# Performance work log

Hardware: AMD Instinct MI355X
Metric: run time of the kernel (lower is better)

Reference implementation:

```python
import jax, jax.numpy as jnp
import numpy as np

PATCH = 7
STRIDE = 1
PDIM = 3 * PATCH * PATCH  # 147


def _extract_patches(im):
    # torch.nn.Unfold(kernel=7, stride=1): output [b, c*k*k, L] with channel-major
    # ordering, which matches conv_general_dilated_patches' channel-major layout.
    b = im.shape[0]
    p = jax.lax.conv_general_dilated_patches(
        im, filter_shape=(PATCH, PATCH), window_strides=(STRIDE, STRIDE), padding='VALID'
    )  # [b, 147, h', w']
    p = p.reshape(b, PDIM, -1).transpose(0, 2, 1)  # [b, L, 147]
    # normalize_patch='mean': std_mean over ALL dims, only the mean is subtracted
    return p - p.mean()


def setup_inputs() -> dict:
    key = jax.random.key(0)
    k1, k2, k3, k4, k5 = jax.random.split(key, 5)
    B, C, H, W = 16, 3, 128, 128
    L = ((H - PATCH) // STRIDE + 1) ** 2  # 14884
    n_samples, n_proj = 4096, 128
    x = jax.random.normal(k1, (B, C, H, W), dtype=jnp.float32)
    y = jax.random.normal(k2, (B, C, H, W), dtype=jnp.float32)
    # faithful quirk: sample_same_locations=True re-draws a fresh permutation for y
    idx_x = jax.random.permutation(k3, L)[:n_samples].astype(jnp.int32)
    idx_y = jax.random.permutation(k4, L)[:n_samples].astype(jnp.int32)
    proj = jax.random.normal(k5, (PDIM, n_proj), dtype=jnp.float32)
    proj = proj / jnp.linalg.norm(proj, axis=0, keepdims=True)  # unit-norm slices
    return {"x": x, "y": y, "proj": proj, "idx_x": idx_x, "idx_y": idx_y}


def reference(x, y, proj, idx_x, idx_y):
    xp = _extract_patches(x)[:, idx_x]  # [b, n, 147]
    yp = _extract_patches(y)[:, idx_y]  # [b, n, 147]
    # SWD dist_metric, vectorized over the batch dim (replaces the Python loop):
    # project patches onto random unit directions, sort along the sample axis,
    # mean absolute difference of sorted projections.
    px = jnp.sort(jnp.einsum('bnd,dp->bnp', xp, proj), axis=1)  # [b, n, P]
    py = jnp.sort(jnp.einsum('bnd,dp->bnp', yp, proj), axis=1)
    per_sample = jnp.mean(jnp.abs(px - py), axis=(1, 2))  # [b]
    return per_sample.mean()  # batch_reduction='mean'
```

## Files before the change

### kernel.cpp

```cpp
#include <hip/hip_runtime.h>
#include <cstddef>
#include <cstdint>

#define BATCH 16
#define CHAN 3
#define HH 128
#define WW 128
#define PATCHK 7
#define HP 122
#define PDIM 147
#define NSAMP 4096
#define NPROJ 128
#define IMG_PIX (CHAN*HH*WW)
#define TOT_PIX (BATCH*IMG_PIX)
#define COUNT_D ((double)BATCH*HP*HP*PDIM)

__global__ __launch_bounds__(256)
void k_wsum(const float* __restrict__ x, const float* __restrict__ y,
            double* __restrict__ outx, double* __restrict__ outy) {
  float sx = 0.f, sy = 0.f;
  const int stride = gridDim.x * blockDim.x;
  for (int e = blockIdx.x * blockDim.x + threadIdx.x; e < TOT_PIX; e += stride) {
    int j = e & (WW - 1);
    int i = (e >> 7) & (HH - 1);
    int wi = min(i, HP - 1) - max(0, i - (PATCHK - 1)) + 1;
    int wj = min(j, HP - 1) - max(0, j - (PATCHK - 1)) + 1;
    float w = (float)(wi * wj);
    sx = fmaf(x[e], w, sx);
    sy = fmaf(y[e], w, sy);
  }
  __shared__ float rx[256], ry[256];
  const int tid = threadIdx.x;
  rx[tid] = sx; ry[tid] = sy;
  __syncthreads();
  for (int off = 128; off; off >>= 1) {
    if (tid < off) { rx[tid] += rx[tid + off]; ry[tid] += ry[tid + off]; }
    __syncthreads();
  }
  if (tid == 0) { outx[blockIdx.x] = (double)rx[0]; outy[blockIdx.x] = (double)ry[0]; }
}

__global__ void k_meandiff(const double* __restrict__ px, const double* __restrict__ py,
                           double* __restrict__ dmean) {
  __shared__ double s[256];
  const int tid = threadIdx.x;
  s[tid] = px[tid] - py[tid];
  __syncthreads();
  for (int off = 128; off; off >>= 1) {
    if (tid < off) s[tid] += s[tid + off];
    __syncthreads();
  }
  if (tid == 0) dmean[0] = s[0] / COUNT_D;
}

__global__ void k_colsum(const float* __restrict__ proj, float* __restrict__ sp) {
  const int p = threadIdx.x;
  float s = 0.f;
  for (int d = 0; d < PDIM; ++d) s += proj[d * NPROJ + p];
  sp[p] = s;
}

#define TM 64
#define ASTR (TM + 1)
__global__ __launch_bounds__(256)
void k_proj(const float* __restrict__ x, const float* __restrict__ y,
            const float* __restrict__ proj,
            const int* __restrict__ idx_x, const int* __restrict__ idx_y,
            float* __restrict__ PX, float* __restrict__ PY) {
  __shared__ float As[PDIM * ASTR];

  const int z = blockIdx.z;
  const float* im = z ? y : x;
  const int* idx = z ? idx_y : idx_x;
  float* dst = z ? PY : PX;
  const int b = blockIdx.y;
  const int nbase = blockIdx.x * TM;
  const int tid = threadIdx.x;

  const float* imb = im + b * IMG_PIX;
  for (int e = tid; e < TM * PDIM; e += 256) {
    int n = e / PDIM;
    int d = e - n * PDIM;
    int l = idx[nbase + n];
    int h0 = l / HP;
    int w0 = l - h0 * HP;
    int c  = d / 49;
    int r  = d - c * 49;
    int kh = r / 7;
    int kw = r - kh * 7;
    As[d * ASTR + n] = imb[(c * HH + h0 + kh) * WW + w0 + kw];
  }
  __syncthreads();

  const int lane = tid & 63;
  const int w = __builtin_amdgcn_readfirstlane(tid >> 6);
  const float* bp = proj + w * 32;

  float acc[32];
#pragma unroll
  for (int pp = 0; pp < 32; ++pp) acc[pp] = 0.f;

  for (int k = 0; k < PDIM; ++k) {
    const float a = As[k * ASTR + lane];
#pragma unroll
    for (int pp = 0; pp < 32; ++pp)
      acc[pp] = fmaf(a, bp[k * NPROJ + pp], acc[pp]);
  }

#pragma unroll
  for (int pp = 0; pp < 32; ++pp)
    dst[(size_t)(b * NPROJ + w * 32 + pp) * NSAMP + nbase + lane] = acc[pp];
}

#define CSWAP(a, b, u) { float _lo = fminf(a, b), _hi = fmaxf(a, b); \
                         (a) = (u) ? _lo : _hi; (b) = (u) ? _hi : _lo; }

#define PHASEA(v, u8) do { \
  CSWAP(v[0], v[1], true);  CSWAP(v[2], v[3], false); \
  CSWAP(v[4], v[5], true);  CSWAP(v[6], v[7], false); \
  CSWAP(v[0], v[2], true);  CSWAP(v[1], v[3], true);  \
  CSWAP(v[4], v[6], false); CSWAP(v[5], v[7], false); \
  CSWAP(v[0], v[1], true);  CSWAP(v[2], v[3], true);  \
  CSWAP(v[4], v[5], false); CSWAP(v[6], v[7], false); \
  CSWAP(v[0], v[4], u8); CSWAP(v[1], v[5], u8); \
  CSWAP(v[2], v[6], u8); CSWAP(v[3], v[7], u8); \
  CSWAP(v[0], v[2], u8); CSWAP(v[1], v[3], u8); \
  CSWAP(v[4], v[6], u8); CSWAP(v[5], v[7], u8); \
  CSWAP(v[0], v[1], u8); CSWAP(v[2], v[3], u8); \
  CSWAP(v[4], v[5], u8); CSWAP(v[6], v[7], u8); } while (0)

#define REG3(v, up) do { \
  CSWAP(v[0], v[4], up); CSWAP(v[1], v[5], up); \
  CSWAP(v[2], v[6], up); CSWAP(v[3], v[7], up); \
  CSWAP(v[0], v[2], up); CSWAP(v[1], v[3], up); \
  CSWAP(v[4], v[6], up); CSWAP(v[5], v[7], up); \
  CSWAP(v[0], v[1], up); CSWAP(v[2], v[3], up); \
  CSWAP(v[4], v[5], up); CSWAP(v[6], v[7], up); } while (0)

template <int DL>
__device__ __forceinline__ void shufstage(float (&vx)[8], float (&vy)[8],
                                          int t, bool up) {
  const bool keepLo = (((t & DL) == 0) == up);
#pragma unroll
  for (int r = 0; r < 8; ++r) {
    float ox = __shfl_xor(vx[r], DL, 64);
    vx[r] = keepLo ? fminf(vx[r], ox) : fmaxf(vx[r], ox);
    float oy = __shfl_xor(vy[r], DL, 64);
    vy[r] = keepLo ? fminf(vy[r], oy) : fmaxf(vy[r], oy);
  }
}

template <int K>
__device__ __forceinline__ void merge_inwave(float (&vx)[8], float (&vy)[8],
                                             int t, int ib) {
  const bool up = ((ib & K) == 0);
  if (K / 2 >= 256) shufstage<32>(vx, vy, t, up);
  if (K / 2 >= 128) shufstage<16>(vx, vy, t, up);
  if (K / 2 >= 64)  shufstage<8>(vx, vy, t, up);
  if (K / 2 >= 32)  shufstage<4>(vx, vy, t, up);
  if (K / 2 >= 16)  shufstage<2>(vx, vy, t, up);
  if (K / 2 >= 8)   shufstage<1>(vx, vy, t, up);
  REG3(vx, up);
  REG3(vy, up);
}

__device__ __forceinline__ void lds_stage(float (&vx)[8], float (&vy)[8],
                                          float* lx, float* ly, int t, int dl, bool up) {
  ((float4*)lx)[t * 2]     = make_float4(vx[0], vx[1], vx[2], vx[3]);
  ((float4*)lx)[t * 2 + 1] = make_float4(vx[4], vx[5], vx[6], vx[7]);
  ((float4*)ly)[t * 2]     = make_float4(vy[0], vy[1], vy[2], vy[3]);
  ((float4*)ly)[t * 2 + 1] = make_float4(vy[4], vy[5], vy[6], vy[7]);
  __syncthreads();
  const int pt = (t ^ dl) * 2;
  float4 ox0 = ((const float4*)lx)[pt], ox1 = ((const float4*)lx)[pt + 1];
  float4 oy0 = ((const float4*)ly)[pt], oy1 = ((const float4*)ly)[pt + 1];
  const bool kl = (((t & dl) == 0) == up);
  vx[0] = kl ? fminf(vx[0], ox0.x) : fmaxf(vx[0], ox0.x);
  vx[1] = kl ? fminf(vx[1], ox0.y) : fmaxf(vx[1], ox0.y);
  vx[2] = kl ? fminf(vx[2], ox0.z) : fmaxf(vx[2], ox0.z);
  vx[3] = kl ? fminf(vx[3], ox0.w) : fmaxf(vx[3], ox0.w);
  vx[4] = kl ? fminf(vx[4], ox1.x) : fmaxf(vx[4], ox1.x);
  vx[5] = kl ? fminf(vx[5], ox1.y) : fmaxf(vx[5], ox1.y);
  vx[6] = kl ? fminf(vx[6], ox1.z) : fmaxf(vx[6], ox1.z);
  vx[7] = kl ? fminf(vx[7], ox1.w) : fmaxf(vx[7], ox1.w);
  vy[0] = kl ? fminf(vy[0], oy0.x) : fmaxf(vy[0], oy0.x);
  vy[1] = kl ? fminf(vy[1], oy0.y) : fmaxf(vy[1], oy0.y);
  vy[2] = kl ? fminf(vy[2], oy0.z) : fmaxf(vy[2], oy0.z);
  vy[3] = kl ? fminf(vy[3], oy0.w) : fmaxf(vy[3], oy0.w);
  vy[4] = kl ? fminf(vy[4], oy1.x) : fmaxf(vy[4], oy1.x);
  vy[5] = kl ? fminf(vy[5], oy1.y) : fmaxf(vy[5], oy1.y);
  vy[6] = kl ? fminf(vy[6], oy1.z) : fmaxf(vy[6], oy1.z);
  vy[7] = kl ? fminf(vy[7], oy1.w) : fmaxf(vy[7], oy1.w);
  __syncthreads();
}

__global__ __launch_bounds__(512)
void k_sortdiff(const float* __restrict__ PX, const float* __restrict__ PY,
                const float* __restrict__ sp, const double* __restrict__ dmean,
                float* __restrict__ bsum) {
  __shared__ float lx[NSAMP];
  __shared__ float ly[NSAMP];
  __shared__ float red[8];
  const int bp = blockIdx.x;
  const int p = bp & (NPROJ - 1);
  const int t = threadIdx.x;
  const int ib = t * 8;

  float vx[8], vy[8];
  {
    const float4* rx = (const float4*)(PX + (size_t)bp * NSAMP) + t * 2;
    const float4* ry = (const float4*)(PY + (size_t)bp * NSAMP) + t * 2;
    float4 x0 = rx[0], x1 = rx[1], y0 = ry[0], y1 = ry[1];
    vx[0]=x0.x; vx[1]=x0.y; vx[2]=x0.z; vx[3]=x0.w;
    vx[4]=x1.x; vx[5]=x1.y; vx[6]=x1.z; vx[7]=x1.w;
    vy[0]=y0.x; vy[1]=y0.y; vy[2]=y0.z; vy[3]=y0.w;
    vy[4]=y1.x; vy[5]=y1.y; vy[6]=y1.z; vy[7]=y1.w;
  }

  {
    const bool u8 = ((t & 1) == 0);
    PHASEA(vx, u8);
    PHASEA(vy, u8);
  }

  merge_inwave<16>(vx, vy, t, ib);
  merge_inwave<32>(vx, vy, t, ib);
  merge_inwave<64>(vx, vy, t, ib);
  merge_inwave<128>(vx, vy, t, ib);
  merge_inwave<256>(vx, vy, t, ib);
  merge_inwave<512>(vx, vy, t, ib);

  {
    const bool up = ((ib & 1024) == 0);
    lds_stage(vx, vy, lx, ly, t, 512 >> 3, up);
    merge_inwave<1024>(vx, vy, t, ib);
  }
  {
    const bool up = ((ib & 2048) == 0);
    lds_stage(vx, vy, lx, ly, t, 1024 >> 3, up);
    lds_stage(vx, vy, lx, ly, t, 512 >> 3, up);
    merge_inwave<2048>(vx, vy, t, ib);
  }
  {
    const bool up = true;
    lds_stage(vx, vy, lx, ly, t, 2048 >> 3, up);
    lds_stage(vx, vy, lx, ly, t, 1024 >> 3, up);
    lds_stage(vx, vy, lx, ly, t, 512 >> 3, up);
    merge_inwave<4096>(vx, vy, t, ib);
  }

  const float delta = (float)(dmean[0]) * sp[p];
  float s = 0.f;
#pragma unroll
  for (int r = 0; r < 8; ++r) s += fabsf(vx[r] - vy[r] - delta);

#pragma unroll
  for (int o = 1; o < 64; o <<= 1) s += __shfl_xor(s, o, 64);
  if ((t & 63) == 0) red[t >> 6] = s;
  __syncthreads();
  if (t == 0) {
    float tot = 0.f;
#pragma unroll
    for (int i = 0; i < 8; ++i) tot += red[i];
    bsum[bp] = tot;
  }
}

__global__ void k_final(const float* __restrict__ bsum, float* __restrict__ out) {
  __shared__ double s[256];
  const int tid = threadIdx.x;
  double v = 0.0;
  for (int q = tid; q < BATCH * NPROJ; q += 256) v += (double)bsum[q];
  s[tid] = v;
  __syncthreads();
  for (int off = 128; off; off >>= 1) {
    if (tid < off) s[tid] += s[tid + off];
    __syncthreads();
  }
  if (tid == 0) out[0] = (float)(s[0] / ((double)NSAMP * NPROJ * BATCH));
}

extern "C" void kernel_launch(void* const* d_in, const int* in_sizes, int n_in,
                              void* d_out, int out_size, void* d_ws, size_t ws_size,
                              hipStream_t stream) {
  const float* x    = (const float*)d_in[0];
  const float* y    = (const float*)d_in[1];
  const float* proj = (const float*)d_in[2];
  const int* idx_x  = (const int*)d_in[3];
  const int* idx_y  = (const int*)d_in[4];
  float* out = (float*)d_out;

  char* ws = (char*)d_ws;
  double* pAx   = (double*)(ws + 0);
  double* pAy   = (double*)(ws + 2048);
  double* dmean = (double*)(ws + 4096);
  float*  sp    = (float*)(ws + 4160);
  float*  bsum  = (float*)(ws + 8192);
  float*  PX    = (float*)(ws + 16384);
  float*  PY    = PX + (size_t)BATCH * NPROJ * NSAMP;

  const size_t need = 16384 + 2ull * BATCH * NPROJ * NSAMP * sizeof(float);
  if (ws_size < need) return;

  k_wsum    <<<256, 256, 0, stream>>>(x, y, pAx, pAy);
  k_meandiff<<<1, 256, 0, stream>>>(pAx, pAy, dmean);
  k_colsum  <<<1, NPROJ, 0, stream>>>(proj, sp);
  k_proj    <<<dim3(NSAMP / TM, BATCH, 2), 256, 0, stream>>>(x, y, proj, idx_x, idx_y, PX, PY);
  k_sortdiff<<<BATCH * NPROJ, 512, 0, stream>>>(PX, PY, sp, dmean, bsum);
  k_final   <<<1, 256, 0, stream>>>(bsum, out);
}
```

Measured before the change: 266.3 us.

## Use sign-flip bitonic sort, DS swizzles, B-register double buffering, fused colsum

The bitonic sort now handles descending runs by XOR-flipping sign bits before and after each merge stage, so every compare-swap becomes a plain min/max instead of a direction-dependent select. Shuffles with lane distance 16 or less use ds_swizzle instead of the generic shfl_xor. The projection GEMM double-buffers the projection-row loads in registers, and the column-sum kernel is folded into the mean-difference kernel to save a launch. The sign-flip trick relies on an order-reversing bit mapping, and the larger register arrays could lower occupancy in k_proj.

```diff
diff --git a/kernel.cpp b/kernel.cpp
--- a/kernel.cpp
+++ b/kernel.cpp
@@ -41,27 +41,35 @@
 }
 
 __global__ void k_meandiff(const double* __restrict__ px, const double* __restrict__ py,
-                           double* __restrict__ dmean) {
-  __shared__ double s[256];
+                           double* __restrict__ dmean,
+                           const float* __restrict__ proj, float* __restrict__ sp) {
   const int tid = threadIdx.x;
-  s[tid] = px[tid] - py[tid];
+  if (tid < NPROJ) {
+    float s = 0.f;
+    for (int d = 0; d < PDIM; ++d) s += proj[d * NPROJ + tid];
+    sp[tid] = s;
+  }
+  __shared__ double sd[256];
+  sd[tid] = px[tid] - py[tid];
   __syncthreads();
   for (int off = 128; off; off >>= 1) {
-    if (tid < off) s[tid] += s[tid + off];
+    if (tid < off) sd[tid] += sd[tid + off];
     __syncthreads();
   }
-  if (tid == 0) dmean[0] = s[0] / COUNT_D;
-}
-
-__global__ void k_colsum(const float* __restrict__ proj, float* __restrict__ sp) {
-  const int p = threadIdx.x;
-  float s = 0.f;
-  for (int d = 0; d < PDIM; ++d) s += proj[d * NPROJ + p];
-  sp[p] = s;
+  if (tid == 0) dmean[0] = sd[0] / COUNT_D;
 }
 
 #define TM 64
 #define ASTR (TM + 1)
+__device__ __forceinline__ void loadb(float (&dst)[32], const float* bp, int kk) {
+#pragma unroll
+  for (int pp = 0; pp < 32; ++pp) dst[pp] = bp[kk * NPROJ + pp];
+}
+__device__ __forceinline__ void fma32(float a, const float (&b)[32], float (&acc)[32]) {
+#pragma unroll
+  for (int pp = 0; pp < 32; ++pp) acc[pp] = fmaf(a, b[pp], acc[pp]);
+}
+
 __global__ __launch_bounds__(256)
 void k_proj(const float* __restrict__ x, const float* __restrict__ y,
             const float* __restrict__ proj,
@@ -100,11 +108,19 @@
 #pragma unroll
   for (int pp = 0; pp < 32; ++pp) acc[pp] = 0.f;
 
-  for (int k = 0; k < PDIM; ++k) {
-    const float a = As[k * ASTR + lane];
-#pragma unroll
-    for (int pp = 0; pp < 32; ++pp)
-      acc[pp] = fmaf(a, bp[k * NPROJ + pp], acc[pp]);
+  float bA[32], bB[32];
+  loadb(bA, bp, 0);
+  for (int k = 0; k + 2 < PDIM; k += 2) {
+    loadb(bB, bp, k + 1);
+    const float a0 = As[k * ASTR + lane];
+    const float a1 = As[(k + 1) * ASTR + lane];
+    fma32(a0, bA, acc);
+    loadb(bA, bp, k + 2);
+    fma32(a1, bB, acc);
+  }
+  {
+    const float a = As[146 * ASTR + lane];
+    fma32(a, bA, acc);
   }
 
 #pragma unroll
@@ -112,60 +128,51 @@
     dst[(size_t)(b * NPROJ + w * 32 + pp) * NSAMP + nbase + lane] = acc[pp];
 }
 
-#define CSWAP(a, b, u) { float _lo = fminf(a, b), _hi = fmaxf(a, b); \
-                         (a) = (u) ? _lo : _hi; (b) = (u) ? _hi : _lo; }
-
-#define PHASEA(v, u8) do { \
-  CSWAP(v[0], v[1], true);  CSWAP(v[2], v[3], false); \
-  CSWAP(v[4], v[5], true);  CSWAP(v[6], v[7], false); \
-  CSWAP(v[0], v[2], true);  CSWAP(v[1], v[3], true);  \
-  CSWAP(v[4], v[6], false); CSWAP(v[5], v[7], false); \
-  CSWAP(v[0], v[1], true);  CSWAP(v[2], v[3], true);  \
-  CSWAP(v[4], v[5], false); CSWAP(v[6], v[7], false); \
-  CSWAP(v[0], v[4], u8); CSWAP(v[1], v[5], u8); \
-  CSWAP(v[2], v[6], u8); CSWAP(v[3], v[7], u8); \
-  CSWAP(v[0], v[2], u8); CSWAP(v[1], v[3], u8); \
-  CSWAP(v[4], v[6], u8); CSWAP(v[5], v[7], u8); \
-  CSWAP(v[0], v[1], u8); CSWAP(v[2], v[3], u8); \
-  CSWAP(v[4], v[5], u8); CSWAP(v[6], v[7], u8); } while (0)
-
-#define REG3(v, up) do { \
-  CSWAP(v[0], v[4], up); CSWAP(v[1], v[5], up); \
-  CSWAP(v[2], v[6], up); CSWAP(v[3], v[7], up); \
-  CSWAP(v[0], v[2], up); CSWAP(v[1], v[3], up); \
-  CSWAP(v[4], v[6], up); CSWAP(v[5], v[7], up); \
-  CSWAP(v[0], v[1], up); CSWAP(v[2], v[3], up); \
-  CSWAP(v[4], v[5], up); CSWAP(v[6], v[7], up); } while (0)
+__device__ __forceinline__ float xorf(float v, unsigned m) {
+  return __int_as_float(__float_as_int(v) ^ (int)m);
+}
+#define CSW(a, b) { float _t = fminf(a, b); b = fmaxf(a, b); a = _t; }
+
+#define SORT8A(v) do { \
+  CSW(v[0],v[1]); CSW(v[3],v[2]); CSW(v[4],v[5]); CSW(v[7],v[6]); \
+  CSW(v[0],v[2]); CSW(v[1],v[3]); CSW(v[6],v[4]); CSW(v[7],v[5]); \
+  CSW(v[0],v[1]); CSW(v[2],v[3]); CSW(v[5],v[4]); CSW(v[7],v[6]); \
+  CSW(v[0],v[4]); CSW(v[1],v[5]); CSW(v[2],v[6]); CSW(v[3],v[7]); \
+  CSW(v[0],v[2]); CSW(v[1],v[3]); CSW(v[4],v[6]); CSW(v[5],v[7]); \
+  CSW(v[0],v[1]); CSW(v[2],v[3]); CSW(v[4],v[5]); CSW(v[6],v[7]); } while (0)
+
+#define REG3A(v) do { \
+  CSW(v[0],v[4]); CSW(v[1],v[5]); CSW(v[2],v[6]); CSW(v[3],v[7]); \
+  CSW(v[0],v[2]); CSW(v[1],v[3]); CSW(v[4],v[6]); CSW(v[5],v[7]); \
+  CSW(v[0],v[1]); CSW(v[2],v[3]); CSW(v[4],v[5]); CSW(v[6],v[7]); } while (0)
+
+#define FLIP8(v, m) { v[0]=xorf(v[0],m); v[1]=xorf(v[1],m); v[2]=xorf(v[2],m); \
+  v[3]=xorf(v[3],m); v[4]=xorf(v[4],m); v[5]=xorf(v[5],m); v[6]=xorf(v[6],m); \
+  v[7]=xorf(v[7],m); }
 
 template <int DL>
-__device__ __forceinline__ void shufstage(float (&vx)[8], float (&vy)[8],
-                                          int t, bool up) {
-  const bool keepLo = (((t & DL) == 0) == up);
+__device__ __forceinline__ float swzxor(float v) {
+  if constexpr (DL <= 16) {
+    return __int_as_float(
+        __builtin_amdgcn_ds_swizzle(__float_as_int(v), (DL << 10) | 0x1F));
+  } else {
+    return __shfl_xor(v, DL, 64);
+  }
+}
+
+template <int DL>
+__device__ __forceinline__ void shufxy(float (&vx)[8], float (&vy)[8], bool keepLo) {
 #pragma unroll
   for (int r = 0; r < 8; ++r) {
-    float ox = __shfl_xor(vx[r], DL, 64);
+    float ox = swzxor<DL>(vx[r]);
     vx[r] = keepLo ? fminf(vx[r], ox) : fmaxf(vx[r], ox);
-    float oy = __shfl_xor(vy[r], DL, 64);
+    float oy = swzxor<DL>(vy[r]);
     vy[r] = keepLo ? fminf(vy[r], oy) : fmaxf(vy[r], oy);
   }
 }
 
-template <int K>
-__device__ __forceinline__ void merge_inwave(float (&vx)[8], float (&vy)[8],
-                                             int t, int ib) {
-  const bool up = ((ib & K) == 0);
-  if (K / 2 >= 256) shufstage<32>(vx, vy, t, up);
-  if (K / 2 >= 128) shufstage<16>(vx, vy, t, up);
-  if (K / 2 >= 64)  shufstage<8>(vx, vy, t, up);
-  if (K / 2 >= 32)  shufstage<4>(vx, vy, t, up);
-  if (K / 2 >= 16)  shufstage<2>(vx, vy, t, up);
-  if (K / 2 >= 8)   shufstage<1>(vx, vy, t, up);
-  REG3(vx, up);
-  REG3(vy, up);
-}
-
 __device__ __forceinline__ void lds_stage(float (&vx)[8], float (&vy)[8],
-                                          float* lx, float* ly, int t, int dl, bool up) {
+                                          float* lx, float* ly, int t, int dl, bool kl) {
   ((float4*)lx)[t * 2]     = make_float4(vx[0], vx[1], vx[2], vx[3]);
   ((float4*)lx)[t * 2 + 1] = make_float4(vx[4], vx[5], vx[6], vx[7]);
   ((float4*)ly)[t * 2]     = make_float4(vy[0], vy[1], vy[2], vy[3]);
@@ -174,7 +181,6 @@
   const int pt = (t ^ dl) * 2;
   float4 ox0 = ((const float4*)lx)[pt], ox1 = ((const float4*)lx)[pt + 1];
   float4 oy0 = ((const float4*)ly)[pt], oy1 = ((const float4*)ly)[pt + 1];
-  const bool kl = (((t & dl) == 0) == up);
   vx[0] = kl ? fminf(vx[0], ox0.x) : fmaxf(vx[0], ox0.x);
   vx[1] = kl ? fminf(vx[1], ox0.y) : fmaxf(vx[1], ox0.y);
   vx[2] = kl ? fminf(vx[2], ox0.z) : fmaxf(vx[2], ox0.z);
@@ -203,8 +209,23 @@
   __shared__ float red[8];
   const int bp = blockIdx.x;
   const int p = bp & (NPROJ - 1);
-  const int t = threadIdx.x;
-  const int ib = t * 8;
+  const unsigned t = threadIdx.x;
+
+  const unsigned g = t ^ (t >> 1);
+  const unsigned mA    = (t & 1u)   << 31;
+  const unsigned dA16  = (g & 1u)   << 31;
+  const unsigned d16   = (g & 2u)   << 30;
+  const unsigned d32   = (g & 4u)   << 29;
+  const unsigned d64   = (g & 8u)   << 28;
+  const unsigned d128  = (g & 16u)  << 27;
+  const unsigned d256  = (g & 32u)  << 26;
+  const unsigned d512  = (g & 64u)  << 25;
+  const unsigned d1024 = (g & 128u) << 24;
+  const unsigned d2048 = (t & 256u) << 23;
+
+  const bool k1  = (t & 1u)  == 0, k2  = (t & 2u)  == 0, k4 = (t & 4u) == 0;
+  const bool k8  = (t & 8u)  == 0, k16 = (t & 16u) == 0, k32 = (t & 32u) == 0;
+  const bool kl64 = (t & 64u) == 0, kl128 = (t & 128u) == 0, kl256 = (t & 256u) == 0;
 
   float vx[8], vy[8];
   {
@@ -217,37 +238,44 @@
     vy[4]=y1.x; vy[5]=y1.y; vy[6]=y1.z; vy[7]=y1.w;
   }
 
-  {
-    const bool u8 = ((t & 1) == 0);
-    PHASEA(vx, u8);
-    PHASEA(vy, u8);
-  }
-
-  merge_inwave<16>(vx, vy, t, ib);
-  merge_inwave<32>(vx, vy, t, ib);
-  merge_inwave<64>(vx, vy, t, ib);
-  merge_inwave<128>(vx, vy, t, ib);
-  merge_inwave<256>(vx, vy, t, ib);
-  merge_inwave<512>(vx, vy, t, ib);
-
-  {
-    const bool up = ((ib & 1024) == 0);
-    lds_stage(vx, vy, lx, ly, t, 512 >> 3, up);
-    merge_inwave<1024>(vx, vy, t, ib);
-  }
-  {
-    const bool up = ((ib & 2048) == 0);
-    lds_stage(vx, vy, lx, ly, t, 1024 >> 3, up);
-    lds_stage(vx, vy, lx, ly, t, 512 >> 3, up);
-    merge_inwave<2048>(vx, vy, t, ib);
-  }
-  {
-    const bool up = true;
-    lds_stage(vx, vy, lx, ly, t, 2048 >> 3, up);
-    lds_stage(vx, vy, lx, ly, t, 1024 >> 3, up);
-    lds_stage(vx, vy, lx, ly, t, 512 >> 3, up);
-    merge_inwave<4096>(vx, vy, t, ib);
-  }
+  FLIP8(vx, mA); FLIP8(vy, mA);
+  SORT8A(vx); SORT8A(vy);
+  FLIP8(vx, dA16); FLIP8(vy, dA16);
+
+  shufxy<1>(vx, vy, k1); REG3A(vx); REG3A(vy);
+  FLIP8(vx, d16); FLIP8(vy, d16);
+  shufxy<2>(vx, vy, k2); shufxy<1>(vx, vy, k1); REG3A(vx); REG3A(vy);
+  FLIP8(vx, d32); FLIP8(vy, d32);
+  shufxy<4>(vx, vy, k4); shufxy<2>(vx, vy, k2); shufxy<1>(vx, vy, k1);
+  REG3A(vx); REG3A(vy);
+  FLIP8(vx, d64); FLIP8(vy, d64);
+  shufxy<8>(vx, vy, k8); shufxy<4>(vx, vy, k4); shufxy<2>(vx, vy, k2);
+  shufxy<1>(vx, vy, k1); REG3A(vx); REG3A(vy);
+  FLIP8(vx, d128); FLIP8(vy, d128);
+  shufxy<16>(vx, vy, k16); shufxy<8>(vx, vy, k8); shufxy<4>(vx, vy, k4);
+  shufxy<2>(vx, vy, k2); shufxy<1>(vx, vy, k1); REG3A(vx); REG3A(vy);
+  FLIP8(vx, d256); FLIP8(vy, d256);
+  shufxy<32>(vx, vy, k32); shufxy<16>(vx, vy, k16); shufxy<8>(vx, vy, k8);
+  shufxy<4>(vx, vy, k4); shufxy<2>(vx, vy, k2); shufxy<1>(vx, vy, k1);
+  REG3A(vx); REG3A(vy);
+  FLIP8(vx, d512); FLIP8(vy, d512);
+  lds_stage(vx, vy, lx, ly, (int)t, 64, kl64);
+  shufxy<32>(vx, vy, k32); shufxy<16>(vx, vy, k16); shufxy<8>(vx, vy, k8);
+  shufxy<4>(vx, vy, k4); shufxy<2>(vx, vy, k2); shufxy<1>(vx, vy, k1);
+  REG3A(vx); REG3A(vy);
+  FLIP8(vx, d1024); FLIP8(vy, d1024);
+  lds_stage(vx, vy, lx, ly, (int)t, 128, kl128);
+  lds_stage(vx, vy, lx, ly, (int)t, 64, kl64);
+  shufxy<32>(vx, vy, k32); shufxy<16>(vx, vy, k16); shufxy<8>(vx, vy, k8);
+  shufxy<4>(vx, vy, k4); shufxy<2>(vx, vy, k2); shufxy<1>(vx, vy, k1);
+  REG3A(vx); REG3A(vy);
+  FLIP8(vx, d2048); FLIP8(vy, d2048);
+  lds_stage(vx, vy, lx, ly, (int)t, 256, kl256);
+  lds_stage(vx, vy, lx, ly, (int)t, 128, kl128);
+  lds_stage(vx, vy, lx, ly, (int)t, 64, kl64);
+  shufxy<32>(vx, vy, k32); shufxy<16>(vx, vy, k16); shufxy<8>(vx, vy, k8);
+  shufxy<4>(vx, vy, k4); shufxy<2>(vx, vy, k2); shufxy<1>(vx, vy, k1);
+  REG3A(vx); REG3A(vy);
 
   const float delta = (float)(dmean[0]) * sp[p];
   float s = 0.f;
@@ -256,7 +284,7 @@
 
 #pragma unroll
   for (int o = 1; o < 64; o <<= 1) s += __shfl_xor(s, o, 64);
-  if ((t & 63) == 0) red[t >> 6] = s;
+  if ((t & 63u) == 0) red[t >> 6] = s;
   __syncthreads();
   if (t == 0) {
     float tot = 0.f;
@@ -303,8 +331,7 @@
   if (ws_size < need) return;
 
   k_wsum    <<<256, 256, 0, stream>>>(x, y, pAx, pAy);
-  k_meandiff<<<1, 256, 0, stream>>>(pAx, pAy, dmean);
-  k_colsum  <<<1, NPROJ, 0, stream>>>(proj, sp);
+  k_meandiff<<<1, 256, 0, stream>>>(pAx, pAy, dmean, proj, sp);
   k_proj    <<<dim3(NSAMP / TM, BATCH, 2), 256, 0, stream>>>(x, y, proj, idx_x, idx_y, PX, PY);
   k_sortdiff<<<BATCH * NPROJ, 512, 0, stream>>>(PX, PY, sp, dmean, bsum);
   k_final   <<<1, 256, 0, stream>>>(bsum, out);
```

Result: faster. 251.1 us (-5.7%).
